# Kernel optimization log

Measured on AMD Instinct MI355X. Metric: run time of the kernel, lower is better.

The kernel has to match this reference:

```python
import jax, jax.numpy as jnp
import numpy as np

B, N, F = 1, 100000, 128
H, C = 8, F // 8          # heads, per-head channels (GATv2: out_channels = hidden//heads)
E = 1600000               # edges
FF = 4 * F                # feedforward hidden
NEG_SLOPE = 0.2           # PyG GATv2 default negative_slope
EPS = 1e-5


def layer_norm(x, g, b):
    mu = jnp.mean(x, axis=-1, keepdims=True)
    var = jnp.mean((x - mu) ** 2, axis=-1, keepdims=True)
    return (x - mu) / jnp.sqrt(var + EPS) * g + b


def setup_inputs() -> dict:
    key = jax.random.key(0)
    ks = jax.random.split(key, 16)
    s = 1.0 / np.sqrt(F)
    return {
        "x": jax.random.normal(ks[0], (B, N, F), dtype=jnp.float32),
        "edge_index": jax.random.randint(ks[1], (2, E), 0, B * N, dtype=jnp.int32),
        # GATv2Conv params (lin_l -> source/x_j, lin_r -> target/x_i), stored [in, out]
        "Wl": jax.random.normal(ks[2], (F, H * C), dtype=jnp.float32) * s,
        "bl": jnp.zeros((H * C,), dtype=jnp.float32),
        "Wr": jax.random.normal(ks[3], (F, H * C), dtype=jnp.float32) * s,
        "br": jnp.zeros((H * C,), dtype=jnp.float32),
        "att": jax.random.normal(ks[4], (H, C), dtype=jnp.float32) * s,
        "bias_gat": jnp.zeros((H * C,), dtype=jnp.float32),
        # LayerNorm1, FFN, LayerNorm2
        "g1": jnp.ones((F,), dtype=jnp.float32),
        "bn1": jnp.zeros((F,), dtype=jnp.float32),
        "W1": jax.random.normal(ks[5], (F, FF), dtype=jnp.float32) * s,
        "bW1": jnp.zeros((FF,), dtype=jnp.float32),
        "W2": jax.random.normal(ks[6], (FF, F), dtype=jnp.float32) * (1.0 / np.sqrt(FF)),
        "bW2": jnp.zeros((F,), dtype=jnp.float32),
        "g2": jnp.ones((F,), dtype=jnp.float32),
        "bn2": jnp.zeros((F,), dtype=jnp.float32),
    }


def reference(x, edge_index, Wl, bl, Wr, br, att, bias_gat,
              g1, bn1, W1, bW1, W2, bW2, g2, bn2):
    # dropout is identity in eval mode
    xf = x.reshape(B * N, F)
    xl = (xf @ Wl + bl).reshape(B * N, H, C)  # source-side transform (x_j)
    xr = (xf @ Wr + br).reshape(B * N, H, C)  # target-side transform (x_i)
    src, dst = edge_index[0], edge_index[1]

    # GATv2 edge scores: e = a^T LeakyReLU(x_i + x_j)
    xj = xl[src]                               # [E, H, C]
    s_e = jax.nn.leaky_relu(xr[dst] + xj, NEG_SLOPE)
    e = jnp.einsum('ehc,hc->eh', s_e, att)     # [E, H]

    # segment softmax over incoming edges of each target node
    m = jax.lax.stop_gradient(jax.ops.segment_max(e, dst, num_segments=B * N))
    ex = jnp.exp(e - m[dst])
    denom = jax.ops.segment_sum(ex, dst, num_segments=B * N)
    alpha = ex / denom[dst]                    # [E, H]

    # scatter-add aggregation, heads concatenated, + bias
    out = jax.ops.segment_sum(xj * alpha[..., None], dst, num_segments=B * N)
    h = (out.reshape(B * N, H * C) + bias_gat).reshape(B, N, F)

    # FFN block with pre-norm residual, then final norm
    ff = layer_norm(h, g1, bn1)
    ff = jax.nn.silu(ff @ W1 + bW1) @ W2 + bW2
    h = h + ff
    return layer_norm(h, g2, bn2)
```

## Files before the change

### kernel.cpp

```cpp
#include <hip/hip_runtime.h>
#include <math.h>

#define FDIM 128
#define NEG_SLOPE 0.2f
#define LN_EPS 1e-5f


__global__ void k_zero(int* __restrict__ p, int n) {
    int i = blockIdx.x * blockDim.x + threadIdx.x;
    if (i < n) p[i] = 0;
}

__global__ void k_deg(const int* __restrict__ ei, int E, int* __restrict__ deg) {
    int i = blockIdx.x * blockDim.x + threadIdx.x;
    if (i < E) atomicAdd(&deg[ei[E + i]], 1);
}

__global__ __launch_bounds__(1024) void k_scan(const int* __restrict__ deg,
                                               int* __restrict__ offs, int N) {
    __shared__ int tl[1024];
    int tid = threadIdx.x;
    int chunk = (N + 1023) >> 10;
    int s = tid * chunk;
    int e = s + chunk; if (e > N) e = N;
    int sum = 0;
    for (int i = s; i < e; ++i) sum += deg[i];
    tl[tid] = sum;
    __syncthreads();
    for (int off = 1; off < 1024; off <<= 1) {
        int v = (tid >= off) ? tl[tid - off] : 0;
        __syncthreads();
        tl[tid] += v;
        __syncthreads();
    }
    int run = tl[tid] - sum;
    for (int i = s; i < e; ++i) { offs[i] = run; run += deg[i]; }
    if (tid == 1023) offs[N] = run;
}

__global__ void k_fill(const int* __restrict__ ei, int E, const int* __restrict__ offs,
                       int* __restrict__ cur, int* __restrict__ csr_src) {
    int i = blockIdx.x * blockDim.x + threadIdx.x;
    if (i < E) {
        int dst = ei[E + i];
        int p = offs[dst] + atomicAdd(&cur[dst], 1);
        csr_src[p] = ei[i];
    }
}

__global__ __launch_bounds__(256) void k_xlxr(const float* __restrict__ x,
        const float* __restrict__ Wl, const float* __restrict__ bl,
        const float* __restrict__ Wr, const float* __restrict__ br,
        float* __restrict__ xl, float* __restrict__ xr, int N) {
    __shared__ __align__(16) float xs[32][128];
    int tid = threadIdx.x;
    int row0 = blockIdx.x * 32;
    for (int v = tid; v < 32 * 32; v += 256) {
        int r = v >> 5, c4 = v & 31;
        int gr = row0 + r;
        float4 val = (gr < N) ? ((const float4*)x)[(size_t)gr * 32 + c4]
                              : make_float4(0.f, 0.f, 0.f, 0.f);
        *(float4*)&xs[r][c4 * 4] = val;
    }
    __syncthreads();

    int cg = tid & 63;
    int rg = tid >> 6;
    int j = cg * 4;
    const float* W = (j < 128) ? (Wl + j) : (Wr + (j - 128));
    const float* bp = (j < 128) ? (bl + j) : (br + (j - 128));
    float4 acc[8];
#pragma unroll
    for (int r = 0; r < 8; ++r) acc[r] = make_float4(0.f, 0.f, 0.f, 0.f);

    for (int k = 0; k < 128; ++k) {
        float4 w = *(const float4*)(W + (size_t)k * 128);
#pragma unroll
        for (int r = 0; r < 8; ++r) {
            float s = xs[rg * 8 + r][k];
            acc[r].x += s * w.x; acc[r].y += s * w.y;
            acc[r].z += s * w.z; acc[r].w += s * w.w;
        }
    }
    float4 b = *(const float4*)bp;
    float* outb = (j < 128) ? xl : xr;
    int jj = (j < 128) ? j : (j - 128);
#pragma unroll
    for (int r = 0; r < 8; ++r) {
        int gr = row0 + rg * 8 + r;
        if (gr < N) {
            float4 v = make_float4(acc[r].x + b.x, acc[r].y + b.y,
                                   acc[r].z + b.z, acc[r].w + b.w);
            *(float4*)&outb[(size_t)gr * 128 + jj] = v;
        }
    }
}

#define GAT_UPD(m_, l_, a_, xv_) { \
    float sx_ = xrv.x + xv_.x; \
    float sy_ = xrv.y + xv_.y; \
    sx_ = (sx_ > 0.f) ? sx_ : NEG_SLOPE * sx_; \
    sy_ = (sy_ > 0.f) ? sy_ : NEG_SLOPE * sy_; \
    float p_ = sx_ * av.x + sy_ * av.y; \
    p_ += __shfl_xor(p_, 1); \
    p_ += __shfl_xor(p_, 2); \
    p_ += __shfl_xor(p_, 4); \
    float mn_ = fmaxf(m_, p_); \
    float sc_ = __expf(m_ - mn_); \
    float w_  = __expf(p_ - mn_); \
    l_ = l_ * sc_ + w_; \
    a_.x = a_.x * sc_ + w_ * xv_.x; \
    a_.y = a_.y * sc_ + w_ * xv_.y; \
    m_ = mn_; }

__global__ __launch_bounds__(256) void k_gat(const float* __restrict__ xl,
        const float* __restrict__ xr, const float* __restrict__ att,
        const float* __restrict__ bias,
        const int* __restrict__ offs, const int* __restrict__ csr_src,
        float* __restrict__ h, int N) {
    int wave = threadIdx.x >> 6;
    int lane = threadIdx.x & 63;
    int node = blockIdx.x * 4 + wave;
    if (node >= N) return;

    int c0 = lane * 2;
    float2 xrv = *(const float2*)&xr[(size_t)node * 128 + c0];
    float2 av  = *(const float2*)&att[c0];

    float mA = -3.0e38f, lA = 0.f, mB = -3.0e38f, lB = 0.f;
    float mC = -3.0e38f, lC = 0.f, mD = -3.0e38f, lD = 0.f;
    float2 aA = make_float2(0.f, 0.f), aB = make_float2(0.f, 0.f);
    float2 aC = make_float2(0.f, 0.f), aD = make_float2(0.f, 0.f);

    int e0 = offs[node], e1 = offs[node + 1];
    int i = e0;
    for (; i + 3 < e1; i += 4) {
        int s0 = csr_src[i];
        int s1 = csr_src[i + 1];
        int s2 = csr_src[i + 2];
        int s3 = csr_src[i + 3];
        float2 x0 = *(const float2*)&xl[(size_t)s0 * 128 + c0];
        float2 x1 = *(const float2*)&xl[(size_t)s1 * 128 + c0];
        float2 x2 = *(const float2*)&xl[(size_t)s2 * 128 + c0];
        float2 x3 = *(const float2*)&xl[(size_t)s3 * 128 + c0];
        GAT_UPD(mA, lA, aA, x0);
        GAT_UPD(mB, lB, aB, x1);
        GAT_UPD(mC, lC, aC, x2);
        GAT_UPD(mD, lD, aD, x3);
    }
    for (; i < e1; ++i) {
        int s0 = csr_src[i];
        float2 x0 = *(const float2*)&xl[(size_t)s0 * 128 + c0];
        GAT_UPD(mA, lA, aA, x0);
    }

    float mn1 = fmaxf(mA, mB);
    float sA = __expf(mA - mn1), sB = __expf(mB - mn1);
    float l1 = lA * sA + lB * sB;
    float2 a1 = make_float2(aA.x * sA + aB.x * sB, aA.y * sA + aB.y * sB);

    float mn2 = fmaxf(mC, mD);
    float sC = __expf(mC - mn2), sD = __expf(mD - mn2);
    float l2 = lC * sC + lD * sD;
    float2 a2 = make_float2(aC.x * sC + aD.x * sD, aC.y * sC + aD.y * sD);

    float mn = fmaxf(mn1, mn2);
    float s1m = __expf(mn1 - mn), s2m = __expf(mn2 - mn);
    float l = l1 * s1m + l2 * s2m;
    float2 acc = make_float2(a1.x * s1m + a2.x * s2m,
                             a1.y * s1m + a2.y * s2m);

    float inv = (l > 0.f) ? (1.f / l) : 0.f;
    float2 bv = *(const float2*)&bias[c0];
    float2 o = make_float2(acc.x * inv + bv.x, acc.y * inv + bv.y);
    *(float2*)&h[(size_t)node * 128 + c0] = o;
}

__global__ __launch_bounds__(256) void k_ffn(const float* __restrict__ h,
        const float* __restrict__ g1, const float* __restrict__ bn1,
        const float* __restrict__ W1, const float* __restrict__ bW1,
        const float* __restrict__ W2, const float* __restrict__ bW2,
        const float* __restrict__ g2, const float* __restrict__ bn2,
        float* __restrict__ out, int N) {
    __shared__ __align__(16) float hs[16][128];
    __shared__ __align__(16) float ts[16][128];
    __shared__ __align__(16) float us[16][512];
    int tid = threadIdx.x;
    int row0 = blockIdx.x * 16;

    for (int v = tid; v < 512; v += 256) {
        int r = v >> 5, c4 = v & 31;
        int gr = row0 + r;
        float4 val = (gr < N) ? ((const float4*)h)[(size_t)gr * 32 + c4]
                              : make_float4(0.f, 0.f, 0.f, 0.f);
        *(float4*)&hs[r][c4 * 4] = val;
    }
    __syncthreads();

    {
        int g = tid >> 4, l16 = tid & 15;
        int c = l16 * 8;
        float4 a = *(float4*)&hs[g][c];
        float4 b = *(float4*)&hs[g][c + 4];
        float sum = a.x + a.y + a.z + a.w + b.x + b.y + b.z + b.w;
        float sq  = a.x*a.x + a.y*a.y + a.z*a.z + a.w*a.w
                  + b.x*b.x + b.y*b.y + b.z*b.z + b.w*b.w;
#pragma unroll
        for (int msk = 1; msk < 16; msk <<= 1) {
            sum += __shfl_xor(sum, msk);
            sq  += __shfl_xor(sq,  msk);
        }
        float mu = sum * (1.f / 128.f);
        float var = sq * (1.f / 128.f) - mu * mu;
        float rstd = rsqrtf(var + LN_EPS);
#pragma unroll
        for (int u = 0; u < 8; ++u) {
            float xv = hs[g][c + u];
            ts[g][c + u] = (xv - mu) * rstd * g1[c + u] + bn1[c + u];
        }
    }
    __syncthreads();

    {
        float acc0[16], acc1[16];
#pragma unroll
        for (int r = 0; r < 16; ++r) { acc0[r] = 0.f; acc1[r] = 0.f; }
        int j0 = tid, j1 = tid + 256;
        for (int k4 = 0; k4 < 32; ++k4) {
            int kb = k4 * 4;
            float wA0 = W1[(size_t)(kb + 0) * 512 + j0];
            float wA1 = W1[(size_t)(kb + 1) * 512 + j0];
            float wA2 = W1[(size_t)(kb + 2) * 512 + j0];
            float wA3 = W1[(size_t)(kb + 3) * 512 + j0];
            float wB0 = W1[(size_t)(kb + 0) * 512 + j1];
            float wB1 = W1[(size_t)(kb + 1) * 512 + j1];
            float wB2 = W1[(size_t)(kb + 2) * 512 + j1];
            float wB3 = W1[(size_t)(kb + 3) * 512 + j1];
#pragma unroll
            for (int r = 0; r < 16; ++r) {
                float4 tv = *(const float4*)&ts[r][kb];
                acc0[r] += tv.x * wA0 + tv.y * wA1 + tv.z * wA2 + tv.w * wA3;
                acc1[r] += tv.x * wB0 + tv.y * wB1 + tv.z * wB2 + tv.w * wB3;
            }
        }
        float b0 = bW1[j0], b1 = bW1[j1];
#pragma unroll
        for (int r = 0; r < 16; ++r) {
            float v0 = acc0[r] + b0;
            float v1 = acc1[r] + b1;
            us[r][j0] = v0 * __builtin_amdgcn_rcpf(1.f + __expf(-v0));
            us[r][j1] = v1 * __builtin_amdgcn_rcpf(1.f + __expf(-v1));
        }
    }
    __syncthreads();

    {
        int j = tid & 127, rh = tid >> 7;
        float acc[8];
#pragma unroll
        for (int r = 0; r < 8; ++r) acc[r] = 0.f;
        for (int k4 = 0; k4 < 128; ++k4) {
            int kb = k4 * 4;
            float w0 = W2[(size_t)(kb + 0) * 128 + j];
            float w1 = W2[(size_t)(kb + 1) * 128 + j];
            float w2 = W2[(size_t)(kb + 2) * 128 + j];
            float w3 = W2[(size_t)(kb + 3) * 128 + j];
#pragma unroll
            for (int r = 0; r < 8; ++r) {
                float4 uv = *(const float4*)&us[rh * 8 + r][kb];
                acc[r] += uv.x * w0 + uv.y * w1 + uv.z * w2 + uv.w * w3;
            }
        }
        float bb = bW2[j];
#pragma unroll
        for (int r = 0; r < 8; ++r) {
            ts[rh * 8 + r][j] = acc[r] + bb + hs[rh * 8 + r][j];
        }
    }
    __syncthreads();

    {
        int g = tid >> 4, l16 = tid & 15;
        int c = l16 * 8;
        float4 a = *(float4*)&ts[g][c];
        float4 b = *(float4*)&ts[g][c + 4];
        float sum = a.x + a.y + a.z + a.w + b.x + b.y + b.z + b.w;
        float sq  = a.x*a.x + a.y*a.y + a.z*a.z + a.w*a.w
                  + b.x*b.x + b.y*b.y + b.z*b.z + b.w*b.w;
#pragma unroll
        for (int msk = 1; msk < 16; msk <<= 1) {
            sum += __shfl_xor(sum, msk);
            sq  += __shfl_xor(sq,  msk);
        }
        float mu = sum * (1.f / 128.f);
        float var = sq * (1.f / 128.f) - mu * mu;
        float rstd = rsqrtf(var + LN_EPS);
        int gr = row0 + g;
        if (gr < N) {
#pragma unroll
            for (int u = 0; u < 8; ++u) {
                float xv = ts[g][c + u];
                out[(size_t)gr * 128 + c + u] =
                    (xv - mu) * rstd * g2[c + u] + bn2[c + u];
            }
        }
    }
}

extern "C" void kernel_launch(void* const* d_in, const int* in_sizes, int n_in,
                              void* d_out, int out_size, void* d_ws, size_t ws_size,
                              hipStream_t stream) {
    const float* x        = (const float*)d_in[0];
    const int*   ei       = (const int*)  d_in[1];
    const float* Wl       = (const float*)d_in[2];
    const float* bl       = (const float*)d_in[3];
    const float* Wr       = (const float*)d_in[4];
    const float* br       = (const float*)d_in[5];
    const float* att      = (const float*)d_in[6];
    const float* bias_gat = (const float*)d_in[7];
    const float* g1       = (const float*)d_in[8];
    const float* bn1      = (const float*)d_in[9];
    const float* W1       = (const float*)d_in[10];
    const float* bW1      = (const float*)d_in[11];
    const float* W2       = (const float*)d_in[12];
    const float* bW2      = (const float*)d_in[13];
    const float* g2       = (const float*)d_in[14];
    const float* bn2      = (const float*)d_in[15];

    int N = in_sizes[0] / 128;
    int E = in_sizes[1] / 2;

    char* w = (char*)d_ws;
    float* xl  = (float*)w; w += (size_t)N * 128 * 4;
    float* xr  = (float*)w; w += (size_t)N * 128 * 4;
    float* hb  = (float*)w; w += (size_t)N * 128 * 4;
    int* offs  = (int*)w;   w += (size_t)(N + 1) * 4;
    int* deg   = (int*)w;   w += (size_t)N * 4;
    int* csr   = (int*)w;   w += (size_t)E * 4;
    float* out = (float*)d_out;

    int eb = (E + 255) / 256;
    int nb = (N + 255) / 256;

    k_zero<<<nb, 256, 0, stream>>>(deg, N);
    k_deg<<<eb, 256, 0, stream>>>(ei, E, deg);
    k_scan<<<1, 1024, 0, stream>>>(deg, offs, N);
    k_zero<<<nb, 256, 0, stream>>>(deg, N);
    k_fill<<<eb, 256, 0, stream>>>(ei, E, offs, deg, csr);

    k_xlxr<<<(N + 31) / 32, 256, 0, stream>>>(x, Wl, bl, Wr, br, xl, xr, N);
    k_gat<<<(N + 3) / 4, 256, 0, stream>>>(xl, xr, att, bias_gat, offs, csr, hb, N);
    k_ffn<<<(N + 15) / 16, 256, 0, stream>>>(hb, g1, bn1, W1, bW1, W2, bW2,
                                             g2, bn2, out, N);
}
```

Baseline: 1.212 ms.

## Retile FFN kernel into wave-private row blocks and drop block barriers

The FFN kernel now gives each wave its own four rows for every stage: LayerNorm1, the W1 GEMM with SiLU, the W2 GEMM with residual, and LayerNorm2. Because no wave reads rows another wave wrote, all __syncthreads barriers are removed, and LayerNorm1 takes its input directly from registers. Each thread computes a 4x8 (then 4x2) register tile using vectorized float4/float2 weight loads. The ts buffer is padded to 132 columns to reduce LDS bank conflicts. The trade-off is that each weight load is now reused across 4 rows instead of 16, which raises global and L1 weight traffic per FLOP.

```diff
diff --git a/kernel.cpp b/kernel.cpp
--- a/kernel.cpp
+++ b/kernel.cpp
@@ -183,25 +183,23 @@
         const float* __restrict__ g2, const float* __restrict__ bn2,
         float* __restrict__ out, int N) {
     __shared__ __align__(16) float hs[16][128];
-    __shared__ __align__(16) float ts[16][128];
+    __shared__ __align__(16) float ts[16][132];
     __shared__ __align__(16) float us[16][512];
     int tid = threadIdx.x;
     int row0 = blockIdx.x * 16;
-
-    for (int v = tid; v < 512; v += 256) {
-        int r = v >> 5, c4 = v & 31;
-        int gr = row0 + r;
-        float4 val = (gr < N) ? ((const float4*)h)[(size_t)gr * 32 + c4]
-                              : make_float4(0.f, 0.f, 0.f, 0.f);
-        *(float4*)&hs[r][c4 * 4] = val;
-    }
-    __syncthreads();
+    int wave = tid >> 6, lane = tid & 63;
+    int g = tid >> 4, l16 = tid & 15, c = l16 * 8;
 
     {
-        int g = tid >> 4, l16 = tid & 15;
-        int c = l16 * 8;
-        float4 a = *(float4*)&hs[g][c];
-        float4 b = *(float4*)&hs[g][c + 4];
+        int gr = row0 + g;
+        float4 a = make_float4(0.f, 0.f, 0.f, 0.f);
+        float4 b = make_float4(0.f, 0.f, 0.f, 0.f);
+        if (gr < N) {
+            a = ((const float4*)h)[(size_t)gr * 32 + l16 * 2];
+            b = ((const float4*)h)[(size_t)gr * 32 + l16 * 2 + 1];
+        }
+        *(float4*)&hs[g][c] = a;
+        *(float4*)&hs[g][c + 4] = b;
         float sum = a.x + a.y + a.z + a.w + b.x + b.y + b.z + b.w;
         float sq  = a.x*a.x + a.y*a.y + a.z*a.z + a.w*a.w
                   + b.x*b.x + b.y*b.y + b.z*b.z + b.w*b.w;
@@ -213,75 +211,102 @@
         float mu = sum * (1.f / 128.f);
         float var = sq * (1.f / 128.f) - mu * mu;
         float rstd = rsqrtf(var + LN_EPS);
-#pragma unroll
-        for (int u = 0; u < 8; ++u) {
-            float xv = hs[g][c + u];
-            ts[g][c + u] = (xv - mu) * rstd * g1[c + u] + bn1[c + u];
-        }
-    }
-    __syncthreads();
+        float xv[8] = {a.x, a.y, a.z, a.w, b.x, b.y, b.z, b.w};
+        float o[8];
+#pragma unroll
+        for (int u = 0; u < 8; ++u)
+            o[u] = (xv[u] - mu) * rstd * g1[c + u] + bn1[c + u];
+        *(float4*)&ts[g][c]     = make_float4(o[0], o[1], o[2], o[3]);
+        *(float4*)&ts[g][c + 4] = make_float4(o[4], o[5], o[6], o[7]);
+    }
+
+    int r0 = wave * 4;
+    int c8 = lane * 8;
+
+    float acc[4][8];
+#pragma unroll
+    for (int r = 0; r < 4; ++r)
+#pragma unroll
+        for (int u = 0; u < 8; ++u) acc[r][u] = 0.f;
+
+    for (int k4 = 0; k4 < 32; ++k4) {
+        int kb = k4 * 4;
+        float4 t4[4];
+        t4[0] = *(const float4*)&ts[r0 + 0][kb];
+        t4[1] = *(const float4*)&ts[r0 + 1][kb];
+        t4[2] = *(const float4*)&ts[r0 + 2][kb];
+        t4[3] = *(const float4*)&ts[r0 + 3][kb];
+        const float* tv = (const float*)t4;
+#pragma unroll
+        for (int kk = 0; kk < 4; ++kk) {
+            const float* wr = W1 + (size_t)(kb + kk) * 512 + c8;
+            float4 wa = *(const float4*)wr;
+            float4 wb = *(const float4*)(wr + 4);
+#pragma unroll
+            for (int r = 0; r < 4; ++r) {
+                float t = tv[r * 4 + kk];
+                acc[r][0] += t * wa.x; acc[r][1] += t * wa.y;
+                acc[r][2] += t * wa.z; acc[r][3] += t * wa.w;
+                acc[r][4] += t * wb.x; acc[r][5] += t * wb.y;
+                acc[r][6] += t * wb.z; acc[r][7] += t * wb.w;
+            }
+        }
+    }
 
     {
-        float acc0[16], acc1[16];
-#pragma unroll
-        for (int r = 0; r < 16; ++r) { acc0[r] = 0.f; acc1[r] = 0.f; }
-        int j0 = tid, j1 = tid + 256;
-        for (int k4 = 0; k4 < 32; ++k4) {
-            int kb = k4 * 4;
-            float wA0 = W1[(size_t)(kb + 0) * 512 + j0];
-            float wA1 = W1[(size_t)(kb + 1) * 512 + j0];
-            float wA2 = W1[(size_t)(kb + 2) * 512 + j0];
-            float wA3 = W1[(size_t)(kb + 3) * 512 + j0];
-            float wB0 = W1[(size_t)(kb + 0) * 512 + j1];
-            float wB1 = W1[(size_t)(kb + 1) * 512 + j1];
-            float wB2 = W1[(size_t)(kb + 2) * 512 + j1];
-            float wB3 = W1[(size_t)(kb + 3) * 512 + j1];
-#pragma unroll
-            for (int r = 0; r < 16; ++r) {
-                float4 tv = *(const float4*)&ts[r][kb];
-                acc0[r] += tv.x * wA0 + tv.y * wA1 + tv.z * wA2 + tv.w * wA3;
-                acc1[r] += tv.x * wB0 + tv.y * wB1 + tv.z * wB2 + tv.w * wB3;
+        float4 b1a = *(const float4*)&bW1[c8];
+        float4 b1b = *(const float4*)&bW1[c8 + 4];
+        float bb[8] = {b1a.x, b1a.y, b1a.z, b1a.w, b1b.x, b1b.y, b1b.z, b1b.w};
+#pragma unroll
+        for (int r = 0; r < 4; ++r) {
+            float o[8];
+#pragma unroll
+            for (int u = 0; u < 8; ++u) {
+                float v = acc[r][u] + bb[u];
+                o[u] = v * __builtin_amdgcn_rcpf(1.f + __expf(-v));
             }
-        }
-        float b0 = bW1[j0], b1 = bW1[j1];
-#pragma unroll
-        for (int r = 0; r < 16; ++r) {
-            float v0 = acc0[r] + b0;
-            float v1 = acc1[r] + b1;
-            us[r][j0] = v0 * __builtin_amdgcn_rcpf(1.f + __expf(-v0));
-            us[r][j1] = v1 * __builtin_amdgcn_rcpf(1.f + __expf(-v1));
-        }
-    }
-    __syncthreads();
+            *(float4*)&us[r0 + r][c8]     = make_float4(o[0], o[1], o[2], o[3]);
+            *(float4*)&us[r0 + r][c8 + 4] = make_float4(o[4], o[5], o[6], o[7]);
+        }
+    }
+
+    int c2 = lane * 2;
+    float acc2[4][2];
+#pragma unroll
+    for (int r = 0; r < 4; ++r) { acc2[r][0] = 0.f; acc2[r][1] = 0.f; }
+
+    for (int k4 = 0; k4 < 128; ++k4) {
+        int kb = k4 * 4;
+        float4 u4[4];
+        u4[0] = *(const float4*)&us[r0 + 0][kb];
+        u4[1] = *(const float4*)&us[r0 + 1][kb];
+        u4[2] = *(const float4*)&us[r0 + 2][kb];
+        u4[3] = *(const float4*)&us[r0 + 3][kb];
+        const float* uv = (const float*)u4;
+#pragma unroll
+        for (int kk = 0; kk < 4; ++kk) {
+            float2 wv = *(const float2*)&W2[(size_t)(kb + kk) * 128 + c2];
+#pragma unroll
+            for (int r = 0; r < 4; ++r) {
+                float u = uv[r * 4 + kk];
+                acc2[r][0] += u * wv.x;
+                acc2[r][1] += u * wv.y;
+            }
+        }
+    }
 
     {
-        int j = tid & 127, rh = tid >> 7;
-        float acc[8];
-#pragma unroll
-        for (int r = 0; r < 8; ++r) acc[r] = 0.f;
-        for (int k4 = 0; k4 < 128; ++k4) {
-            int kb = k4 * 4;
-            float w0 = W2[(size_t)(kb + 0) * 128 + j];
-            float w1 = W2[(size_t)(kb + 1) * 128 + j];
-            float w2 = W2[(size_t)(kb + 2) * 128 + j];
-            float w3 = W2[(size_t)(kb + 3) * 128 + j];
-#pragma unroll
-            for (int r = 0; r < 8; ++r) {
-                float4 uv = *(const float4*)&us[rh * 8 + r][kb];
-                acc[r] += uv.x * w0 + uv.y * w1 + uv.z * w2 + uv.w * w3;
-            }
-        }
-        float bb = bW2[j];
-#pragma unroll
-        for (int r = 0; r < 8; ++r) {
-            ts[rh * 8 + r][j] = acc[r] + bb + hs[rh * 8 + r][j];
-        }
-    }
-    __syncthreads();
+        float2 b2 = *(const float2*)&bW2[c2];
+#pragma unroll
+        for (int r = 0; r < 4; ++r) {
+            int row = r0 + r;
+            float2 hres = *(const float2*)&hs[row][c2];
+            ts[row][c2]     = acc2[r][0] + b2.x + hres.x;
+            ts[row][c2 + 1] = acc2[r][1] + b2.y + hres.y;
+        }
+    }
 
     {
-        int g = tid >> 4, l16 = tid & 15;
-        int c = l16 * 8;
         float4 a = *(float4*)&ts[g][c];
         float4 b = *(float4*)&ts[g][c + 4];
         float sum = a.x + a.y + a.z + a.w + b.x + b.y + b.z + b.w;
@@ -297,11 +322,11 @@
         float rstd = rsqrtf(var + LN_EPS);
         int gr = row0 + g;
         if (gr < N) {
+            float xv[8] = {a.x, a.y, a.z, a.w, b.x, b.y, b.z, b.w};
 #pragma unroll
             for (int u = 0; u < 8; ++u) {
-                float xv = ts[g][c + u];
                 out[(size_t)gr * 128 + c + u] =
-                    (xv - mu) * rstd * g2[c + u] + bn2[c + u];
+                    (xv[u] - mu) * rstd * g2[c + u] + bn2[c + u];
             }
         }
     }
```

Result: no change. 1.218 ms (+0.5%).
